# Optimization experiments

Measured on AMD Instinct MI355X. Metric: run time of the kernel, lower is better.

## Reference

```python
import jax, jax.numpy as jnp
import numpy as np

DIM = 1024
DEPTH = 4
HEADS = 16
DHEAD = 64
INNER = HEADS * DHEAD  # 1024
FF = 4 * DIM           # 4096
SCALE = DHEAD ** -0.5
LS_INIT = 0.1          # LayerScale init_eps for depth <= 18


def _layernorm(x, w, b):
    mu = jnp.mean(x, axis=-1, keepdims=True)
    var = jnp.mean((x - mu) ** 2, axis=-1, keepdims=True)
    return (x - mu) / jnp.sqrt(var + 1e-5) * w + b


def setup_inputs() -> dict:
    key = jax.random.key(0)
    ks = jax.random.split(key, 6)
    s = 0.02
    return {
        "x": jax.random.normal(ks[0], (2, 1024, DIM), dtype=jnp.float32),
        "ln1_w": jnp.ones((DEPTH, DIM), jnp.float32),
        "ln1_b": jnp.zeros((DEPTH, DIM), jnp.float32),
        "w_qkv": jax.random.normal(ks[1], (DEPTH, DIM, 3 * INNER), jnp.float32) * s,
        "w_out": jax.random.normal(ks[2], (DEPTH, INNER, DIM), jnp.float32) * s,
        "b_out": jnp.zeros((DEPTH, DIM), jnp.float32),
        "ls1": jnp.full((DEPTH, DIM), LS_INIT, jnp.float32),
        "ln2_w": jnp.ones((DEPTH, DIM), jnp.float32),
        "ln2_b": jnp.zeros((DEPTH, DIM), jnp.float32),
        "w_ff1": jax.random.normal(ks[3], (DEPTH, DIM, 2 * FF), jnp.float32) * s,
        "b_ff1": jnp.zeros((DEPTH, 2 * FF), jnp.float32),
        "w_ff2": jax.random.normal(ks[4], (DEPTH, FF, DIM), jnp.float32) * s,
        "b_ff2": jnp.zeros((DEPTH, DIM), jnp.float32),
        "ls2": jnp.full((DEPTH, DIM), LS_INIT, jnp.float32),
    }


def _block(x, p):
    (ln1w, ln1b, wqkv, wout, bout, ls1,
     ln2w, ln2b, wff1, bff1, wff2, bff2, ls2) = p
    b, n, _ = x.shape
    # --- PreNorm + Attention (non-causal, no mask) + LayerScale, residual ---
    h = _layernorm(x, ln1w, ln1b)
    qkv = h @ wqkv                                   # [b, n, 3*inner]
    q, k, v = jnp.split(qkv, 3, axis=-1)
    def heads(t):
        return t.reshape(b, n, HEADS, DHEAD).transpose(0, 2, 1, 3)  # b h n d
    q, k, v = heads(q) * SCALE, heads(k), heads(v)
    dots = jnp.einsum("bhid,bhjd->bhij", q, k)       # full O(n^2) scores
    attn = jax.nn.softmax(dots, axis=-1)
    o = jnp.einsum("bhij,bhjd->bhid", attn, v)
    o = o.transpose(0, 2, 1, 3).reshape(b, n, INNER)
    o = o @ wout + bout
    x = x + o * ls1
    # --- PreNorm + GEGLU FeedForward + LayerScale, residual ---
    h = _layernorm(x, ln2w, ln2b)
    u = h @ wff1 + bff1                              # [b, n, 2*FF]
    a, g = jnp.split(u, 2, axis=-1)
    ff = (a * jax.nn.gelu(g, approximate=False)) @ wff2 + bff2
    x = x + ff * ls2
    return x, None


def reference(x, ln1_w, ln1_b, w_qkv, w_out, b_out, ls1,
              ln2_w, ln2_b, w_ff1, b_ff1, w_ff2, b_ff2, ls2):
    ps = (ln1_w, ln1_b, w_qkv, w_out, b_out, ls1,
          ln2_w, ln2_b, w_ff1, b_ff1, w_ff2, b_ff2, ls2)
    out, _ = jax.lax.scan(_block, x, ps)
    return out
```

## Files before the change

kernel.cpp:

```cpp
#include <hip/hip_runtime.h>
#include <cstdint>
#include <cstddef>

typedef __bf16 bf16_t;
typedef __bf16 bf16x8 __attribute__((ext_vector_type(8)));
typedef __bf16 bf16x4 __attribute__((ext_vector_type(4)));
typedef float  f32x4  __attribute__((ext_vector_type(4)));

#define DEV __device__ __forceinline__

static constexpr int   BATCH = 2;
static constexpr int   NTOK  = 1024;
static constexpr int   DIM   = 1024;
static constexpr int   MROWS = BATCH * NTOK;
static constexpr float SCALE = 0.125f;

DEV void load_lds16(const bf16_t* g, bf16_t* s) {
  __builtin_amdgcn_global_load_lds(
      (const __attribute__((address_space(1))) void*)g,
      (__attribute__((address_space(3))) void*)s, 16, 0, 0);
}

DEV float wave_sum(float v) {
#pragma unroll
  for (int m = 1; m < 64; m <<= 1) v += __shfl_xor(v, m, 64);
  return v;
}
DEV float block_sum(float v, float* sb) {
  v = wave_sum(v);
  __syncthreads();
  if ((threadIdx.x & 63) == 0) sb[threadIdx.x >> 6] = v;
  __syncthreads();
  return sb[0] + sb[1] + sb[2] + sb[3];
}

template <int BM, int BN, int WR, int WC, int MODE>
__global__ __launch_bounds__(256) void gemm_bt(
    const bf16_t* __restrict__ A, long sA0, long sA1, int lda,
    const bf16_t* __restrict__ B, long sB0, long sB1, int ldb,
    void* __restrict__ Cv, long sC0, long sC1, int ldc,
    int K, float alpha, const float* __restrict__ bias,
    const float* __restrict__ ls, bf16_t* __restrict__ vtp) {
  constexpr int TM = BM / WR / 16;
  constexpr int TN = BN / WC / 16;
  __shared__ __attribute__((aligned(16))) bf16_t As[BM * 32];
  __shared__ __attribute__((aligned(16))) bf16_t Bs[BN * 32];

  const int tid  = threadIdx.x;
  const int lane = tid & 63, wave = tid >> 6;
  const int z  = blockIdx.z;
  const int zh = z >> 4, zl = z & 15;
  A += (size_t)zh * sA0 + (size_t)zl * sA1;
  B += (size_t)zh * sB0 + (size_t)zl * sB1;

  const int m0 = blockIdx.y * BM, n0 = blockIdx.x * BN;
  const int wm = (wave / WC) * (BM / WR);
  const int wn = (wave % WC) * (BN / WC);
  const int fm = lane & 15, quad = lane >> 4;

  f32x4 acc[TM][TN] = {};

  for (int k0 = 0; k0 < K; k0 += 32) {
#pragma unroll
    for (int c = tid; c < BM * 4; c += 256) {
      const int row = c >> 2, kc = (c & 3) << 3;
      load_lds16(A + (size_t)(m0 + row) * lda + k0 + kc, &As[c * 8]);
    }
#pragma unroll
    for (int c = tid; c < BN * 4; c += 256) {
      const int row = c >> 2, kc = (c & 3) << 3;
      load_lds16(B + (size_t)(n0 + row) * ldb + k0 + kc, &Bs[c * 8]);
    }
    __syncthreads();

    bf16x8 af[TM], bfr[TN];
#pragma unroll
    for (int i = 0; i < TM; ++i)
      af[i] = *(const bf16x8*)&As[(wm + i * 16 + fm) * 32 + quad * 8];
#pragma unroll
    for (int j = 0; j < TN; ++j)
      bfr[j] = *(const bf16x8*)&Bs[(wn + j * 16 + fm) * 32 + quad * 8];
#pragma unroll
    for (int i = 0; i < TM; ++i)
#pragma unroll
      for (int j = 0; j < TN; ++j)
        acc[i][j] = __builtin_amdgcn_mfma_f32_16x16x32_bf16(af[i], bfr[j],
                                                            acc[i][j], 0, 0, 0);
    __syncthreads();
  }

  const size_t coff = (size_t)zh * sC0 + (size_t)zl * sC1;
  if constexpr (MODE == 4) {
    bf16_t* C = (bf16_t*)Cv;
#pragma unroll
    for (int i = 0; i < TM; ++i) {
#pragma unroll
      for (int j = 0; j < TN; ++j) {
        const int col  = n0 + wn + j * 16 + fm;
        const int rowb = m0 + wm + i * 16 + quad * 4;
        if (col < 2048) {
#pragma unroll
          for (int r = 0; r < 4; ++r)
            C[(size_t)(rowb + r) * ldc + col] = (bf16_t)acc[i][j][r];
        } else {
          const int hh = (col - 2048) >> 6, d = (col - 2048) & 63;
#pragma unroll
          for (int r = 0; r < 4; ++r) {
            const int row = rowb + r, bb = row >> 10, tok = row & 1023;
            vtp[((size_t)(bb * 16 + hh) * 64 + d) * 1024 + tok] =
                (bf16_t)acc[i][j][r];
          }
        }
      }
    }
  } else {
#pragma unroll
    for (int i = 0; i < TM; ++i) {
#pragma unroll
      for (int j = 0; j < TN; ++j) {
        const int col  = n0 + wn + j * 16 + fm;
        const int rowb = m0 + wm + i * 16 + quad * 4;
#pragma unroll
        for (int r = 0; r < 4; ++r) {
          const float  v   = acc[i][j][r];
          const size_t idx = coff + (size_t)(rowb + r) * ldc + col;
          if constexpr (MODE == 0) {
            ((bf16_t*)Cv)[idx] = (bf16_t)(v * alpha);
          } else if constexpr (MODE == 1) {
            ((bf16_t*)Cv)[idx] = (bf16_t)(v + bias[col]);
          } else {
            float* C = (float*)Cv;
            C[idx]   = C[idx] + (v + bias[col]) * ls[col];
          }
        }
      }
    }
  }
}

__global__ __launch_bounds__(512, 2) void gemm256_ff1(
    const bf16_t* __restrict__ A,
    const bf16_t* __restrict__ B,
    bf16_t* __restrict__ C,
    const float* __restrict__ bias,
    int K) {
  __shared__ __attribute__((aligned(16))) bf16_t As[2][2][256 * 32];
  __shared__ __attribute__((aligned(16))) bf16_t Bs[2][2][256 * 32];

  const int tid = threadIdx.x, lane = tid & 63, wave = tid >> 6;
  const int wm2 = wave >> 2, wn4 = wave & 3;
  const int fm = lane & 15, quad = lane >> 4;
  const int m0 = blockIdx.y * 256, n0 = blockIdx.x * 256;
  const int NK = K >> 6;

  auto stage = [&](const bf16_t* g, int base, int kt, int kh, bf16_t* s) {
#pragma unroll
    for (int it = 0; it < 2; ++it) {
      const int c = it * 512 + tid, row = c >> 2, kc = (c & 3) << 3;
      load_lds16(g + (size_t)(base + row) * K + kt * 64 + kh * 32 + kc,
                 s + c * 8);
    }
  };

  f32x4 acc[8][4] = {};

  stage(A, m0, 0, 0, &As[0][0][0]);
  stage(B, n0, 0, 0, &Bs[0][0][0]);
  stage(A, m0, 0, 1, &As[0][1][0]);
  stage(B, n0, 0, 1, &Bs[0][1][0]);
  if (NK > 1) {
    stage(A, m0, 1, 0, &As[1][0][0]);
    stage(B, n0, 1, 0, &Bs[1][0][0]);
    stage(A, m0, 1, 1, &As[1][1][0]);
  }
  asm volatile("s_waitcnt vmcnt(6)" ::: "memory");
  __builtin_amdgcn_sched_barrier(0);
  __builtin_amdgcn_s_barrier();

  const int ar = wm2 * 128 + fm;
  const int br = wn4 * 64 + fm;
  const int qo = quad * 8;

  for (int kt = 0; kt < NK; ++kt) {
    const int cur = kt & 1;
    bf16x8 af[8], b0, b1;

#pragma unroll
    for (int m = 0; m < 8; ++m)
      af[m] = *(const bf16x8*)&As[cur][0][(ar + m * 16) * 32 + qo];
    b0 = *(const bf16x8*)&Bs[cur][0][br * 32 + qo];
    b1 = *(const bf16x8*)&Bs[cur][0][(br + 16) * 32 + qo];
    if (kt + 1 < NK) stage(B, n0, kt + 1, 1, &Bs[cur ^ 1][1][0]);
    __builtin_amdgcn_s_barrier();
    __builtin_amdgcn_s_setprio(1);
#pragma unroll
    for (int m = 0; m < 8; ++m) {
      acc[m][0] = __builtin_amdgcn_mfma_f32_16x16x32_bf16(af[m], b0,
                                                          acc[m][0], 0, 0, 0);
      acc[m][1] = __builtin_amdgcn_mfma_f32_16x16x32_bf16(af[m], b1,
                                                          acc[m][1], 0, 0, 0);
    }
    __builtin_amdgcn_s_setprio(0);
    __builtin_amdgcn_s_barrier();

    b0 = *(const bf16x8*)&Bs[cur][0][(br + 32) * 32 + qo];
    b1 = *(const bf16x8*)&Bs[cur][0][(br + 48) * 32 + qo];
    if (kt + 2 < NK) stage(A, m0, kt + 2, 0, &As[cur][0][0]);
    __builtin_amdgcn_s_barrier();
    __builtin_amdgcn_s_setprio(1);
#pragma unroll
    for (int m = 0; m < 8; ++m) {
      acc[m][2] = __builtin_amdgcn_mfma_f32_16x16x32_bf16(af[m], b0,
                                                          acc[m][2], 0, 0, 0);
      acc[m][3] = __builtin_amdgcn_mfma_f32_16x16x32_bf16(af[m], b1,
                                                          acc[m][3], 0, 0, 0);
    }
    __builtin_amdgcn_s_setprio(0);
    __builtin_amdgcn_s_barrier();

#pragma unroll
    for (int m = 0; m < 8; ++m)
      af[m] = *(const bf16x8*)&As[cur][1][(ar + m * 16) * 32 + qo];
    b0 = *(const bf16x8*)&Bs[cur][1][(br + 32) * 32 + qo];
    b1 = *(const bf16x8*)&Bs[cur][1][(br + 48) * 32 + qo];
    if (kt + 2 < NK) stage(B, n0, kt + 2, 0, &Bs[cur][0][0]);
    __builtin_amdgcn_s_barrier();
    __builtin_amdgcn_s_setprio(1);
#pragma unroll
    for (int m = 0; m < 8; ++m) {
      acc[m][2] = __builtin_amdgcn_mfma_f32_16x16x32_bf16(af[m], b0,
                                                          acc[m][2], 0, 0, 0);
      acc[m][3] = __builtin_amdgcn_mfma_f32_16x16x32_bf16(af[m], b1,
                                                          acc[m][3], 0, 0, 0);
    }
    __builtin_amdgcn_s_setprio(0);
    __builtin_amdgcn_s_barrier();

    b0 = *(const bf16x8*)&Bs[cur][1][br * 32 + qo];
    b1 = *(const bf16x8*)&Bs[cur][1][(br + 16) * 32 + qo];
    if (kt + 2 < NK) stage(A, m0, kt + 2, 1, &As[cur][1][0]);
    asm volatile("s_waitcnt vmcnt(6)" ::: "memory");
    __builtin_amdgcn_sched_barrier(0);
    __builtin_amdgcn_s_barrier();
    __builtin_amdgcn_s_setprio(1);
#pragma unroll
    for (int m = 0; m < 8; ++m) {
      acc[m][0] = __builtin_amdgcn_mfma_f32_16x16x32_bf16(af[m], b0,
                                                          acc[m][0], 0, 0, 0);
      acc[m][1] = __builtin_amdgcn_mfma_f32_16x16x32_bf16(af[m], b1,
                                                          acc[m][1], 0, 0, 0);
    }
    __builtin_amdgcn_s_setprio(0);
    __builtin_amdgcn_s_barrier();
  }

#pragma unroll
  for (int m = 0; m < 8; ++m) {
    const int rowb = m0 + wm2 * 128 + m * 16 + quad * 4;
#pragma unroll
    for (int p = 0; p < 2; ++p) {
      const int   cf = ((n0 + wn4 * 64 + p * 32) >> 1) + fm;
      const float ba = bias[cf], bg = bias[4096 + cf];
#pragma unroll
      for (int r = 0; r < 4; ++r) {
        const float a  = acc[m][2 * p][r] + ba;
        const float g  = acc[m][2 * p + 1][r] + bg;
        const float ge = 0.5f * g * (1.f + erff(g * 0.70710678118654752f));
        C[(size_t)(rowb + r) * 4096 + cf] = (bf16_t)(a * ge);
      }
    }
  }
}

__global__ __launch_bounds__(256) void flash_attn(
    const bf16_t* __restrict__ qkv,
    const bf16_t* __restrict__ vT,
    bf16_t* __restrict__ o) {
  constexpr int NT = 128;
  __shared__ __attribute__((aligned(16))) bf16_t Qs[2 * 64 * 32];
  __shared__ __attribute__((aligned(16))) bf16_t Ks[2 * NT * 32];
  __shared__ __attribute__((aligned(16))) bf16_t Vs[4 * 64 * 32];
  __shared__ __attribute__((aligned(16))) bf16_t Ps[4][4 * 16 * 32];

  const int tid = threadIdx.x, lane = tid & 63, wave = tid >> 6;
  const int fm = lane & 15, quad = lane >> 4;
  const int z = blockIdx.y, b = z >> 4, h = z & 15;
  const int q0 = blockIdx.x * 64;
  const bf16_t* qb  = qkv + (size_t)b * 1024 * 3072 + h * 64;
  const bf16_t* kb  = qb + 1024;
  const bf16_t* vtb = vT + (size_t)z * 64 * 1024;

  for (int c = tid; c < 512; c += 256) {
    const int kk = c >> 8, rr = (c >> 2) & 63, ii = c & 3;
    load_lds16(qb + (size_t)(q0 + rr) * 3072 + kk * 32 + ii * 8, &Qs[c * 8]);
  }
  __syncthreads();
  bf16x8 qf[2];
  qf[0] = *(const bf16x8*)&Qs[(wave * 16 + fm) * 32 + quad * 8];
  qf[1] = *(const bf16x8*)&Qs[64 * 32 + (wave * 16 + fm) * 32 + quad * 8];

  float mr[4], lr[4];
  f32x4 oacc[4];
#pragma unroll
  for (int r = 0; r < 4; ++r) { mr[r] = -1e30f; lr[r] = 0.f; }
#pragma unroll
  for (int t = 0; t < 4; ++t) oacc[t] = (f32x4){0.f, 0.f, 0.f, 0.f};

  for (int kv0 = 0; kv0 < 1024; kv0 += NT) {
    __syncthreads();
    for (int c = tid; c < NT * 8; c += 256) {
      const int kk = c >> 9, rr = (c >> 2) & 127, ii = c & 3;
      load_lds16(kb + (size_t)(kv0 + rr) * 3072 + kk * 32 + ii * 8, &Ks[c * 8]);
    }
    for (int c = tid; c < 1024; c += 256) {
      const int tc = c >> 8, rr = (c >> 2) & 63, ii = c & 3;
      load_lds16(vtb + (size_t)rr * 1024 + kv0 + tc * 32 + ii * 8, &Vs[c * 8]);
    }
    __syncthreads();

    f32x4 sc[8];
#pragma unroll
    for (int nt = 0; nt < 8; ++nt) {
      sc[nt] = (f32x4){0.f, 0.f, 0.f, 0.f};
#pragma unroll
      for (int kk = 0; kk < 2; ++kk) {
        const bf16x8 kf =
            *(const bf16x8*)&Ks[kk * NT * 32 + (nt * 16 + fm) * 32 + quad * 8];
        sc[nt] = __builtin_amdgcn_mfma_f32_16x16x32_bf16(qf[kk], kf, sc[nt],
                                                         0, 0, 0);
      }
    }
    float tmax[4] = {-1e30f, -1e30f, -1e30f, -1e30f};
#pragma unroll
    for (int nt = 0; nt < 8; ++nt)
#pragma unroll
      for (int r = 0; r < 4; ++r) {
        sc[nt][r] *= SCALE;
        tmax[r] = fmaxf(tmax[r], sc[nt][r]);
      }
#pragma unroll
    for (int m = 1; m < 16; m <<= 1)
#pragma unroll
      for (int r = 0; r < 4; ++r)
        tmax[r] = fmaxf(tmax[r], __shfl_xor(tmax[r], m, 64));
    float alpha[4], mn[4], ps[4];
#pragma unroll
    for (int r = 0; r < 4; ++r) {
      mn[r]    = fmaxf(mr[r], tmax[r]);
      alpha[r] = __expf(mr[r] - mn[r]);
      mr[r]    = mn[r];
      ps[r]    = 0.f;
    }
#pragma unroll
    for (int nt = 0; nt < 8; ++nt) {
      const int tcol = nt * 16 + fm, kk = tcol >> 5, tw = tcol & 31;
#pragma unroll
      for (int r = 0; r < 4; ++r) {
        const float p = __expf(sc[nt][r] - mn[r]);
        ps[r] += p;
        Ps[wave][kk * 512 + (quad * 4 + r) * 32 + tw] = (bf16_t)p;
      }
    }
#pragma unroll
    for (int m = 1; m < 16; m <<= 1)
#pragma unroll
      for (int r = 0; r < 4; ++r) ps[r] += __shfl_xor(ps[r], m, 64);
#pragma unroll
    for (int r = 0; r < 4; ++r) lr[r] = lr[r] * alpha[r] + ps[r];
#pragma unroll
    for (int t = 0; t < 4; ++t)
#pragma unroll
      for (int r = 0; r < 4; ++r) oacc[t][r] *= alpha[r];
    __builtin_amdgcn_s_waitcnt(0xC07F);
#pragma unroll
    for (int kk = 0; kk < 4; ++kk) {
      const bf16x8 af =
          *(const bf16x8*)&Ps[wave][kk * 512 + fm * 32 + quad * 8];
#pragma unroll
      for (int t = 0; t < 4; ++t) {
        const bf16x8 vf =
            *(const bf16x8*)&Vs[kk * 64 * 32 + (t * 16 + fm) * 32 + quad * 8];
        oacc[t] = __builtin_amdgcn_mfma_f32_16x16x32_bf16(af, vf, oacc[t],
                                                          0, 0, 0);
      }
    }
  }

  const size_t orow0 = (size_t)b * 1024 + q0 + wave * 16 + quad * 4;
#pragma unroll
  for (int t = 0; t < 4; ++t) {
    const int col = h * 64 + t * 16 + fm;
#pragma unroll
    for (int r = 0; r < 4; ++r)
      o[(orow0 + r) * 1024 + col] = (bf16_t)(oacc[t][r] / lr[r]);
  }
}

__global__ __launch_bounds__(256) void transpose_all(
    const float* __restrict__ wqkv, const float* __restrict__ wout,
    const float* __restrict__ wff1, const float* __restrict__ wff2,
    bf16_t* __restrict__ wqkvT, bf16_t* __restrict__ woutT,
    bf16_t* __restrict__ wff1T, bf16_t* __restrict__ wff2T, int l) {
  __shared__ float t[32][33];
  int bx = blockIdx.x;
  const float* W;
  bf16_t*      WT;
  int N, K;
  bool perm = false;
  if (bx < 3072) {
    W = wqkv + (size_t)l * 1024 * 3072; WT = wqkvT; K = 1024; N = 3072;
  } else if (bx < 4096) {
    bx -= 3072;
    W = wout + (size_t)l * 1024 * 1024; WT = woutT; K = 1024; N = 1024;
  } else if (bx < 12288) {
    bx -= 4096;
    W = wff1 + (size_t)l * 1024 * 8192; WT = wff1T; K = 1024; N = 8192;
    perm = true;
  } else {
    bx -= 12288;
    W = wff2 + (size_t)l * 4096 * 1024; WT = wff2T; K = 4096; N = 1024;
  }
  const int nbx = N >> 5;
  const int n0 = (bx % nbx) * 32, k0 = (bx / nbx) * 32;
  const int tx = threadIdx.x & 31, ty = threadIdx.x >> 5;
#pragma unroll
  for (int s = 0; s < 4; ++s)
    t[ty + 8 * s][tx] = W[(size_t)(k0 + ty + 8 * s) * N + n0 + tx];
  __syncthreads();
#pragma unroll
  for (int s = 0; s < 4; ++s) {
    const int n = n0 + ty + 8 * s;
    int r;
    if (perm)
      r = (n < 4096) ? (((n >> 4) << 5) + (n & 15))
                     : ((((n - 4096) >> 4) << 5) + 16 + (n & 15));
    else
      r = n;
    WT[(size_t)r * K + k0 + tx] = (bf16_t)t[tx][ty + 8 * s];
  }
}

__global__ __launch_bounds__(256) void ln_kernel(const float* __restrict__ x,
                                                 const float* __restrict__ w,
                                                 const float* __restrict__ b,
                                                 bf16_t* __restrict__ out) {
  __shared__ float sb[4];
  const int row = blockIdx.x, tid = threadIdx.x;
  const float4 v = ((const float4*)(x + (size_t)row * DIM))[tid];
  float s = v.x + v.y + v.z + v.w;
  s = block_sum(s, sb);
  const float mu = s * (1.f / DIM);
  const float dx = v.x - mu, dy = v.y - mu, dz = v.z - mu, dw = v.w - mu;
  float q = dx * dx + dy * dy + dz * dz + dw * dw;
  q = block_sum(q, sb);
  const float rstd = rsqrtf(q * (1.f / DIM) + 1e-5f);
  const float4 wv = ((const float4*)w)[tid];
  const float4 bv = ((const float4*)b)[tid];
  bf16x4 o;
  o[0] = (bf16_t)(dx * rstd * wv.x + bv.x);
  o[1] = (bf16_t)(dy * rstd * wv.y + bv.y);
  o[2] = (bf16_t)(dz * rstd * wv.z + bv.z);
  o[3] = (bf16_t)(dw * rstd * wv.w + bv.w);
  ((bf16x4*)(out + (size_t)row * DIM))[tid] = o;
}

extern "C" void kernel_launch(void* const* d_in, const int* in_sizes, int n_in,
                              void* d_out, int out_size, void* d_ws,
                              size_t ws_size, hipStream_t stream) {
  const float* x_in = (const float*)d_in[0];
  const float* ln1w = (const float*)d_in[1];
  const float* ln1b = (const float*)d_in[2];
  const float* wqkv = (const float*)d_in[3];
  const float* wout = (const float*)d_in[4];
  const float* bout = (const float*)d_in[5];
  const float* ls1  = (const float*)d_in[6];
  const float* ln2w = (const float*)d_in[7];
  const float* ln2b = (const float*)d_in[8];
  const float* wff1 = (const float*)d_in[9];
  const float* bff1 = (const float*)d_in[10];
  const float* wff2 = (const float*)d_in[11];
  const float* bff2 = (const float*)d_in[12];
  const float* ls2  = (const float*)d_in[13];
  float*       xout = (float*)d_out;

  char*   ws     = (char*)d_ws;
  bf16_t* wqkvT  = (bf16_t*)ws; ws += (size_t)3072 * 1024 * 2;
  bf16_t* woutT  = (bf16_t*)ws; ws += (size_t)1024 * 1024 * 2;
  bf16_t* wff1T  = (bf16_t*)ws; ws += (size_t)8192 * 1024 * 2;
  bf16_t* wff2T  = (bf16_t*)ws; ws += (size_t)1024 * 4096 * 2;
  bf16_t* h_bf   = (bf16_t*)ws; ws += (size_t)MROWS * 1024 * 2;
  bf16_t* qkv_bf = (bf16_t*)ws; ws += (size_t)MROWS * 3072 * 2;
  bf16_t* o_bf   = (bf16_t*)ws; ws += (size_t)MROWS * 1024 * 2;
  bf16_t* vT     = (bf16_t*)ws; ws += (size_t)32 * 64 * 1024 * 2;
  bf16_t* ff_bf  = (bf16_t*)ws; ws += (size_t)MROWS * 4096 * 2;
  if (ws_size < (size_t)(ws - (char*)d_ws)) return;

  hipMemcpyAsync(xout, x_in, (size_t)MROWS * DIM * 4,
                 hipMemcpyDeviceToDevice, stream);

  for (int l = 0; l < 4; ++l) {
    transpose_all<<<dim3(16384), 256, 0, stream>>>(
        wqkv, wout, wff1, wff2, wqkvT, woutT, wff1T, wff2T, l);

    ln_kernel<<<MROWS, 256, 0, stream>>>(xout, ln1w + l * 1024,
                                         ln1b + l * 1024, h_bf);
    gemm_bt<128, 128, 2, 2, 4><<<dim3(24, 16, 1), 256, 0, stream>>>(
        h_bf, 0, 0, 1024, wqkvT, 0, 0, 1024, qkv_bf, 0, 0, 3072, 1024, 1.f,
        nullptr, nullptr, vT);
    flash_attn<<<dim3(16, 32), 256, 0, stream>>>(qkv_bf, vT, o_bf);
    gemm_bt<64, 128, 1, 4, 2><<<dim3(8, 32, 1), 256, 0, stream>>>(
        o_bf, 0, 0, 1024, woutT, 0, 0, 1024, xout, 0, 0, 1024, 1024, 1.f,
        bout + l * 1024, ls1 + l * 1024, nullptr);

    ln_kernel<<<MROWS, 256, 0, stream>>>(xout, ln2w + l * 1024,
                                         ln2b + l * 1024, h_bf);
    gemm256_ff1<<<dim3(32, 8), 512, 0, stream>>>(
        h_bf, wff1T, ff_bf, bff1 + l * 8192, 1024);
    gemm_bt<64, 128, 1, 4, 2><<<dim3(8, 32, 1), 256, 0, stream>>>(
        ff_bf, 0, 0, 4096, wff2T, 0, 0, 4096, xout, 0, 0, 1024, 4096, 1.f,
        bff2 + l * 1024, ls2 + l * 1024, nullptr);
  }
}
```

Measured before the change: 1.134 ms.

## Hoist weight transposes into one launch and split-K residual GEMMs with atomics

All four layers' weights are now transposed to bf16 in a single launch before the layer loop, which replaces four per-layer transpose kernels and needs four times the workspace. The out-projection and FF2 GEMMs are split along K (2 and 4 slices) with a new epilogue mode. That epilogue atomically adds the LayerScale-scaled partial sums, plus the bias from slice zero, into the fp32 residual. This raises the block count for these small-output GEMMs to fill more CUs, at the cost of atomic traffic and a nondeterministic summation order.

```diff
diff --git a/kernel.cpp b/kernel.cpp
--- a/kernel.cpp
+++ b/kernel.cpp
@@ -110,6 +110,23 @@
             vtp[((size_t)(bb * 16 + hh) * 64 + d) * 1024 + tok] =
                 (bf16_t)acc[i][j][r];
           }
+        }
+      }
+    }
+  } else if constexpr (MODE == 5) {
+    float* C = (float*)Cv;
+#pragma unroll
+    for (int i = 0; i < TM; ++i) {
+#pragma unroll
+      for (int j = 0; j < TN; ++j) {
+        const int col  = n0 + wn + j * 16 + fm;
+        const int rowb = m0 + wm + i * 16 + quad * 4;
+        const float lsv = ls[col];
+        const float bl  = (zl == 0) ? bias[col] * lsv : 0.f;
+#pragma unroll
+        for (int r = 0; r < 4; ++r) {
+          const size_t idx = (size_t)(rowb + r) * ldc + col;
+          atomicAdd(&C[idx], acc[i][j][r] * lsv + bl);
         }
       }
     }
@@ -400,25 +417,30 @@
     const float* __restrict__ wqkv, const float* __restrict__ wout,
     const float* __restrict__ wff1, const float* __restrict__ wff2,
     bf16_t* __restrict__ wqkvT, bf16_t* __restrict__ woutT,
-    bf16_t* __restrict__ wff1T, bf16_t* __restrict__ wff2T, int l) {
+    bf16_t* __restrict__ wff1T, bf16_t* __restrict__ wff2T) {
   __shared__ float t[32][33];
+  const int l = blockIdx.y;
   int bx = blockIdx.x;
   const float* W;
   bf16_t*      WT;
   int N, K;
   bool perm = false;
   if (bx < 3072) {
-    W = wqkv + (size_t)l * 1024 * 3072; WT = wqkvT; K = 1024; N = 3072;
+    W = wqkv + (size_t)l * 1024 * 3072;
+    WT = wqkvT + (size_t)l * 3072 * 1024; K = 1024; N = 3072;
   } else if (bx < 4096) {
     bx -= 3072;
-    W = wout + (size_t)l * 1024 * 1024; WT = woutT; K = 1024; N = 1024;
+    W = wout + (size_t)l * 1024 * 1024;
+    WT = woutT + (size_t)l * 1024 * 1024; K = 1024; N = 1024;
   } else if (bx < 12288) {
     bx -= 4096;
-    W = wff1 + (size_t)l * 1024 * 8192; WT = wff1T; K = 1024; N = 8192;
+    W = wff1 + (size_t)l * 1024 * 8192;
+    WT = wff1T + (size_t)l * 8192 * 1024; K = 1024; N = 8192;
     perm = true;
   } else {
     bx -= 12288;
-    W = wff2 + (size_t)l * 4096 * 1024; WT = wff2T; K = 4096; N = 1024;
+    W = wff2 + (size_t)l * 4096 * 1024;
+    WT = wff2T + (size_t)l * 1024 * 4096; K = 4096; N = 1024;
   }
   const int nbx = N >> 5;
   const int n0 = (bx % nbx) * 32, k0 = (bx / nbx) * 32;
@@ -484,10 +506,10 @@
   float*       xout = (float*)d_out;
 
   char*   ws     = (char*)d_ws;
-  bf16_t* wqkvT  = (bf16_t*)ws; ws += (size_t)3072 * 1024 * 2;
-  bf16_t* woutT  = (bf16_t*)ws; ws += (size_t)1024 * 1024 * 2;
-  bf16_t* wff1T  = (bf16_t*)ws; ws += (size_t)8192 * 1024 * 2;
-  bf16_t* wff2T  = (bf16_t*)ws; ws += (size_t)1024 * 4096 * 2;
+  bf16_t* wqkvT  = (bf16_t*)ws; ws += (size_t)4 * 3072 * 1024 * 2;
+  bf16_t* woutT  = (bf16_t*)ws; ws += (size_t)4 * 1024 * 1024 * 2;
+  bf16_t* wff1T  = (bf16_t*)ws; ws += (size_t)4 * 8192 * 1024 * 2;
+  bf16_t* wff2T  = (bf16_t*)ws; ws += (size_t)4 * 1024 * 4096 * 2;
   bf16_t* h_bf   = (bf16_t*)ws; ws += (size_t)MROWS * 1024 * 2;
   bf16_t* qkv_bf = (bf16_t*)ws; ws += (size_t)MROWS * 3072 * 2;
   bf16_t* o_bf   = (bf16_t*)ws; ws += (size_t)MROWS * 1024 * 2;
@@ -498,26 +520,31 @@
   hipMemcpyAsync(xout, x_in, (size_t)MROWS * DIM * 4,
                  hipMemcpyDeviceToDevice, stream);
 
+  transpose_all<<<dim3(16384, 4), 256, 0, stream>>>(
+      wqkv, wout, wff1, wff2, wqkvT, woutT, wff1T, wff2T);
+
   for (int l = 0; l < 4; ++l) {
-    transpose_all<<<dim3(16384), 256, 0, stream>>>(
-        wqkv, wout, wff1, wff2, wqkvT, woutT, wff1T, wff2T, l);
+    const bf16_t* wqkvTl = wqkvT + (size_t)l * 3072 * 1024;
+    const bf16_t* woutTl = woutT + (size_t)l * 1024 * 1024;
+    const bf16_t* wff1Tl = wff1T + (size_t)l * 8192 * 1024;
+    const bf16_t* wff2Tl = wff2T + (size_t)l * 1024 * 4096;
 
     ln_kernel<<<MROWS, 256, 0, stream>>>(xout, ln1w + l * 1024,
                                          ln1b + l * 1024, h_bf);
     gemm_bt<128, 128, 2, 2, 4><<<dim3(24, 16, 1), 256, 0, stream>>>(
-        h_bf, 0, 0, 1024, wqkvT, 0, 0, 1024, qkv_bf, 0, 0, 3072, 1024, 1.f,
+        h_bf, 0, 0, 1024, wqkvTl, 0, 0, 1024, qkv_bf, 0, 0, 3072, 1024, 1.f,
         nullptr, nullptr, vT);
     flash_attn<<<dim3(16, 32), 256, 0, stream>>>(qkv_bf, vT, o_bf);
-    gemm_bt<64, 128, 1, 4, 2><<<dim3(8, 32, 1), 256, 0, stream>>>(
-        o_bf, 0, 0, 1024, woutT, 0, 0, 1024, xout, 0, 0, 1024, 1024, 1.f,
+    gemm_bt<64, 128, 1, 4, 5><<<dim3(8, 32, 2), 256, 0, stream>>>(
+        o_bf, 0, 512, 1024, woutTl, 0, 512, 1024, xout, 0, 0, 1024, 512, 1.f,
         bout + l * 1024, ls1 + l * 1024, nullptr);
 
     ln_kernel<<<MROWS, 256, 0, stream>>>(xout, ln2w + l * 1024,
                                          ln2b + l * 1024, h_bf);
     gemm256_ff1<<<dim3(32, 8), 512, 0, stream>>>(
-        h_bf, wff1T, ff_bf, bff1 + l * 8192, 1024);
-    gemm_bt<64, 128, 1, 4, 2><<<dim3(8, 32, 1), 256, 0, stream>>>(
-        ff_bf, 0, 0, 4096, wff2T, 0, 0, 4096, xout, 0, 0, 1024, 4096, 1.f,
-        bff2 + l * 1024, ls2 + l * 1024, nullptr);
-  }
-}
+        h_bf, wff1Tl, ff_bf, bff1 + l * 8192, 1024);
+    gemm_bt<64, 128, 1, 4, 5><<<dim3(8, 32, 4), 256, 0, stream>>>(
+        ff_bf, 0, 1024, 4096, wff2Tl, 0, 1024, 4096, xout, 0, 0, 1024, 1024,
+        1.f, bff2 + l * 1024, ls2 + l * 1024, nullptr);
+  }
+}
```

Result: faster. 1.109 ms (-2.3%).
